# Kernel tuning notes

Hardware: AMD Instinct MI355X
Metric: run time of the kernel (lower is better)

## Reference

```python
import jax, jax.numpy as jnp
import numpy as np

N = 100000        # num nodes
E = 1200000       # num edges (avg degree 12)
F_IN = 64         # num_features
HID = 64          # hidden_size
NCLS = 40         # num_classes
K = 2             # propagation hops


def setup_inputs() -> dict:
    key = jax.random.key(0)
    k0, k1, k2, k3 = jax.random.split(key, 4)
    x = jax.random.normal(k0, (N, F_IN), dtype=jnp.float32)
    edge_index = jax.random.randint(k1, (2, E), 0, N, dtype=jnp.int32)
    # SGConv's internal Linear (in->hidden) and the classifier fc (hidden->classes)
    W1 = jax.random.normal(k2, (F_IN, HID), dtype=jnp.float32) / np.sqrt(F_IN).astype(np.float32)
    b1 = jnp.zeros((HID,), jnp.float32)
    W2 = jax.random.normal(k3, (HID, NCLS), dtype=jnp.float32) / np.sqrt(HID).astype(np.float32)
    b2 = jnp.zeros((NCLS,), jnp.float32)
    return {"x": x, "edge_index": edge_index, "W1": W1, "b1": b1, "W2": W2, "b2": b2}


def reference(x, edge_index, W1, b1, W2, b2):
    n = x.shape[0]
    # gcn_norm: add self-loops with weight 1, symmetric normalization
    loop = jnp.arange(n, dtype=edge_index.dtype)
    src = jnp.concatenate([edge_index[0], loop])  # message source j
    dst = jnp.concatenate([edge_index[1], loop])  # aggregation target i
    deg = jax.ops.segment_sum(jnp.ones(src.shape, x.dtype), dst, num_segments=n)
    dinv = jnp.where(deg > 0, jax.lax.rsqrt(deg), 0.0)
    norm = dinv[src] * dinv[dst]  # [E+N]
    # K-hop propagation: x_i <- sum_j norm_ij * x_j
    for _ in range(K):
        x = jax.ops.segment_sum(norm[:, None] * x[src], dst, num_segments=n)
    h = jax.nn.relu(x @ W1 + b1)          # SGConv lin + ReLU
    logits = h @ W2 + b2                  # fc
    return jax.nn.log_softmax(logits, axis=1)
```

## Files before the change

### kernel.cpp

```cpp
#include <hip/hip_runtime.h>
#include <math.h>

#define N_NODES 100000
#define BSHIFT 9
#define NBUCK 256
#define CAPSHIFT 13
#define CAP (1 << CAPSHIFT)

typedef unsigned short bfu;
typedef unsigned int uint;
typedef __attribute__((ext_vector_type(8))) short short8v;
typedef __attribute__((ext_vector_type(4))) float f32x4;
typedef __attribute__((ext_vector_type(2))) float f32x2;

__device__ __forceinline__ float bf2f(bfu u) {
    union { uint i; float f; } v; v.i = (uint)u << 16; return v.f;
}
__device__ __forceinline__ bfu f2bf(float f) {
    union { float f_; uint i; } v; v.f_ = f;
    uint r = (v.i + 0x7FFFu + ((v.i >> 16) & 1u)) >> 16;
    return (bfu)r;
}
__device__ __forceinline__ float asf(uint u) {
    union { uint i; float f; } v; v.i = u; return v.f;
}

__global__ __launch_bounds__(256) void bin_edges(const int* __restrict__ src,
                                                 const int* __restrict__ dst,
                                                 int* __restrict__ gcursor,
                                                 uint* __restrict__ binned, int nE) {
    __shared__ int h[NBUCK];
    __shared__ int base[NBUCK];
    int tid = threadIdx.x;
    int start = blockIdx.x * 4096;
    h[tid] = 0;
    __syncthreads();
    int bkt[16], rnk[16];
    #pragma unroll
    for (int u = 0; u < 16; ++u) {
        int e = start + u * 256 + tid;
        bkt[u] = -1;
        if (e < nE) {
            int b = dst[e] >> BSHIFT;
            bkt[u] = b;
            rnk[u] = atomicAdd(&h[b], 1);
        }
    }
    __syncthreads();
    base[tid] = h[tid] ? (tid << CAPSHIFT) + atomicAdd(&gcursor[tid], h[tid]) : 0;
    __syncthreads();
    #pragma unroll
    for (int u = 0; u < 16; ++u) {
        int e = start + u * 256 + tid;
        if (e < nE) {
            uint pk = ((uint)(dst[e] & 511) << 17) | (uint)src[e];
            binned[base[bkt[u]] + rnk[u]] = pk;
        }
    }
}

__global__ __launch_bounds__(512) void build_csr(
    const uint* __restrict__ binned, const int* __restrict__ gcursor,
    int* __restrict__ rowptr, int* __restrict__ rowend,
    float* __restrict__ dinv, int* __restrict__ nbr,
    const float4* __restrict__ x, ushort4* __restrict__ z0, int nN) {
    __shared__ int hist[512];
    __shared__ int cursor[512];
    int b = blockIdx.x, t = threadIdx.x;
    int n0 = b << BSHIFT;
    int nNodes = min(512, nN - n0);
    int base = b << CAPSHIFT;
    int cnt = gcursor[b];
    hist[t] = 0;
    __syncthreads();
    for (int i = t; i < cnt; i += 512)
        atomicAdd(&hist[binned[base + i] >> 17], 1);
    __syncthreads();
    int v = hist[t];
    #pragma unroll
    for (int off = 1; off < 512; off <<= 1) {
        int tv = (t >= off) ? hist[t - off] : 0;
        __syncthreads();
        hist[t] += tv;
        __syncthreads();
    }
    int excl = hist[t] - v;
    float dv = rsqrtf((float)v + 1.0f);
    if (t < nNodes) {
        rowptr[n0 + t] = base + excl;
        rowend[n0 + t] = base + excl + v;
        dinv[n0 + t] = dv;
    }
    cursor[t] = excl;
    __syncthreads();
    ((float*)hist)[t] = dv;
    __syncthreads();
    for (int i = t; i < cnt; i += 512) {
        uint pk = binned[base + i];
        int ld = pk >> 17;
        int pos = atomicAdd(&cursor[ld], 1);
        nbr[base + pos] = (int)(pk & 0x1FFFFu);
    }
    const float4* xr = x + (size_t)n0 * 16;
    ushort4* zr = z0 + (size_t)n0 * 16;
    int totalF4 = nNodes * 16;
    for (int i = t; i < totalF4; i += 512) {
        float w = ((float*)hist)[i >> 4];
        float4 vv = xr[i];
        ushort4 o;
        o.x = f2bf(w * vv.x); o.y = f2bf(w * vv.y);
        o.z = f2bf(w * vv.z); o.w = f2bf(w * vv.w);
        zr[i] = o;
    }
}

template<int PW>
__global__ __launch_bounds__(256, 8) void gather_hop8(
    bfu* __restrict__ out, const bfu* __restrict__ z,
    const int* __restrict__ nbr, const int* __restrict__ rowptr,
    const int* __restrict__ rowend, const float* __restrict__ dinv, int nN) {
    int node = blockIdx.x * 4 + (threadIdx.x >> 6);
    if (node >= nN) return;
    int lane = threadIdx.x & 63;
    int g = lane >> 3, k = lane & 7;
    int beg = rowptr[node], end = rowend[node];

    f32x2 a0 = {0.f, 0.f}, a1 = {0.f, 0.f}, a2 = {0.f, 0.f}, a3 = {0.f, 0.f};

    auto rowload = [&](int s) -> uint4 {
        return reinterpret_cast<const uint4*>(z + (size_t)s * 64)[k];
    };
    auto accum = [&](uint4 v) {
        f32x2 p;
        p.x = asf(v.x << 16); p.y = asf(v.x & 0xFFFF0000u); a0 += p;
        p.x = asf(v.y << 16); p.y = asf(v.y & 0xFFFF0000u); a1 += p;
        p.x = asf(v.z << 16); p.y = asf(v.z & 0xFFFF0000u); a2 += p;
        p.x = asf(v.w << 16); p.y = asf(v.w & 0xFFFF0000u); a3 += p;
    };

    if (g == 0)
        accum(rowload(node));
    int j = beg + g;
    for (; j + 8 < end; j += 16) {
        int i0 = nbr[j], i1 = nbr[j + 8];
        uint4 v0 = rowload(i0);
        uint4 v1 = rowload(i1);
        accum(v0);
        accum(v1);
    }
    if (j < end)
        accum(rowload(nbr[j]));

    float acc[8] = {a0.x, a0.y, a1.x, a1.y, a2.x, a2.y, a3.x, a3.y};
    #pragma unroll
    for (int m = 8; m < 64; m <<= 1)
        #pragma unroll
        for (int i = 0; i < 8; ++i)
            acc[i] += __shfl_xor(acc[i], m);

    if (g == 0) {
        float di = dinv[node];
        float w = (PW == 2) ? di * di : di;
        uint4 o;
        o.x = ((uint)f2bf(acc[1] * w) << 16) | f2bf(acc[0] * w);
        o.y = ((uint)f2bf(acc[3] * w) << 16) | f2bf(acc[2] * w);
        o.z = ((uint)f2bf(acc[5] * w) << 16) | f2bf(acc[4] * w);
        o.w = ((uint)f2bf(acc[7] * w) << 16) | f2bf(acc[6] * w);
        reinterpret_cast<uint4*>(out + (size_t)node * 64)[k] = o;
    }
}

__global__ __launch_bounds__(256) void mlp_mfma(
    float* __restrict__ out, const bfu* __restrict__ zC,
    const float* __restrict__ W1, const float* __restrict__ b1,
    const float* __restrict__ W2, const float* __restrict__ b2,
    int nN, int nTiles) {
    __shared__ short w1t[64 * 72];
    __shared__ short w2t[48 * 72];
    __shared__ short hlds[64 * 72];
    __shared__ float b1s[64];
    __shared__ float b2s[48];

    int tid = threadIdx.x;
    for (int i = tid; i < 64 * 64; i += 256) {
        int k = i >> 6, n = i & 63;
        w1t[n * 72 + k] = (short)f2bf(W1[i]);
    }
    for (int i = tid; i < 48 * 64; i += 256) {
        int k = i / 48, n = i % 48;
        w2t[n * 72 + k] = (short)(n < 40 ? f2bf(W2[k * 40 + n]) : 0);
    }
    if (tid < 64) b1s[tid] = b1[tid];
    if (tid >= 64 && tid < 112) b2s[tid - 64] = (tid - 64 < 40) ? b2[tid - 64] : 0.f;

    int wv = tid >> 6, l = tid & 63;
    int li = l & 15, kg = l >> 4;

    for (int tile = blockIdx.x; tile < nTiles; tile += gridDim.x) {
        int nodebase = tile * 64 + wv * 16;
        int nclamp = min(nodebase + li, nN - 1);

        const short8v* zr = (const short8v*)(zC + (size_t)nclamp * 64);
        short8v a0 = zr[kg];
        short8v a1 = zr[kg + 4];
        __syncthreads();

        f32x4 acc[4];
        #pragma unroll
        for (int nt = 0; nt < 4; ++nt) {
            f32x4 c = {0.f, 0.f, 0.f, 0.f};
            short8v b0 = *(const short8v*)&w1t[(nt * 16 + li) * 72 + kg * 8];
            short8v b1f = *(const short8v*)&w1t[(nt * 16 + li) * 72 + 32 + kg * 8];
            c = __builtin_amdgcn_mfma_f32_16x16x32_bf16(a0, b0, c, 0, 0, 0);
            c = __builtin_amdgcn_mfma_f32_16x16x32_bf16(a1, b1f, c, 0, 0, 0);
            acc[nt] = c;
        }
        #pragma unroll
        for (int nt = 0; nt < 4; ++nt) {
            float bb = b1s[nt * 16 + li];
            #pragma unroll
            for (int r = 0; r < 4; ++r) {
                float v = fmaxf(acc[nt][r] + bb, 0.f);
                hlds[(wv * 16 + kg * 4 + r) * 72 + nt * 16 + li] = (short)f2bf(v);
            }
        }
        __syncthreads();

        const short8v* hp = (const short8v*)&hlds[(wv * 16 + li) * 72];
        short8v ha0 = hp[kg];
        short8v ha1 = hp[kg + 4];
        f32x4 acc2[3];
        #pragma unroll
        for (int nt = 0; nt < 3; ++nt) {
            f32x4 c = {0.f, 0.f, 0.f, 0.f};
            short8v b0 = *(const short8v*)&w2t[(nt * 16 + li) * 72 + kg * 8];
            short8v b1f = *(const short8v*)&w2t[(nt * 16 + li) * 72 + 32 + kg * 8];
            c = __builtin_amdgcn_mfma_f32_16x16x32_bf16(ha0, b0, c, 0, 0, 0);
            c = __builtin_amdgcn_mfma_f32_16x16x32_bf16(ha1, b1f, c, 0, 0, 0);
            acc2[nt] = c;
        }

        float lg[3][4];
        #pragma unroll
        for (int nt = 0; nt < 3; ++nt) {
            float bb = b2s[nt * 16 + li];
            #pragma unroll
            for (int r = 0; r < 4; ++r) lg[nt][r] = acc2[nt][r] + bb;
        }
        bool v2 = (li < 8);
        float mx[4], sm[4];
        #pragma unroll
        for (int r = 0; r < 4; ++r) {
            float m = fmaxf(lg[0][r], lg[1][r]);
            if (v2) m = fmaxf(m, lg[2][r]);
            mx[r] = m;
        }
        #pragma unroll
        for (int off = 1; off < 16; off <<= 1)
            #pragma unroll
            for (int r = 0; r < 4; ++r)
                mx[r] = fmaxf(mx[r], __shfl_xor(mx[r], off));
        #pragma unroll
        for (int r = 0; r < 4; ++r) {
            float s = expf(lg[0][r] - mx[r]) + expf(lg[1][r] - mx[r]);
            if (v2) s += expf(lg[2][r] - mx[r]);
            sm[r] = s;
        }
        #pragma unroll
        for (int off = 1; off < 16; off <<= 1)
            #pragma unroll
            for (int r = 0; r < 4; ++r)
                sm[r] += __shfl_xor(sm[r], off);

        int nb2 = nodebase + kg * 4;
        #pragma unroll
        for (int r = 0; r < 4; ++r) {
            int nd = nb2 + r;
            if (nd < nN) {
                float lse = mx[r] + logf(sm[r]);
                out[(size_t)nd * 40 + li]      = lg[0][r] - lse;
                out[(size_t)nd * 40 + 16 + li] = lg[1][r] - lse;
                if (v2) out[(size_t)nd * 40 + 32 + li] = lg[2][r] - lse;
            }
        }
    }
}

extern "C" void kernel_launch(void* const* d_in, const int* in_sizes, int n_in,
                              void* d_out, int out_size, void* d_ws, size_t ws_size,
                              hipStream_t stream) {
    const float* x   = (const float*)d_in[0];
    const int* eidx  = (const int*)d_in[1];
    const float* W1  = (const float*)d_in[2];
    const float* b1  = (const float*)d_in[3];
    const float* W2  = (const float*)d_in[4];
    const float* b2  = (const float*)d_in[5];
    float* out = (float*)d_out;

    const int nN = N_NODES;
    const int nE = in_sizes[1] / 2;
    const int* src = eidx;
    const int* dst = eidx + nE;
    const int nBk = (nN + 511) >> BSHIFT;

    char* ws = (char*)d_ws;
    size_t off = 0;
    auto alloc = [&](size_t bytes) {
        char* p = ws + off;
        off += (bytes + 255) & ~(size_t)255;
        return p;
    };
    float* dinv    = (float*)alloc((size_t)nN * 4);
    int*   gcursor = (int*)  alloc(NBUCK * 4);
    int*   rowptr  = (int*)  alloc((size_t)nN * 4);
    int*   rowend  = (int*)  alloc((size_t)nN * 4);
    uint*  binned  = (uint*) alloc((size_t)NBUCK * CAP * 4);
    int*   nbr     = (int*)  alloc((size_t)NBUCK * CAP * 4);
    bfu*   z0      = (bfu*)  alloc((size_t)nN * 64 * 2);
    bfu*   zB      = (bfu*)  alloc((size_t)nN * 64 * 2);
    bfu*   zC      = (bfu*)  alloc((size_t)nN * 64 * 2);

    hipMemsetAsync(gcursor, 0, NBUCK * 4, stream);
    bin_edges<<<(nE + 4095) / 4096, 256, 0, stream>>>(src, dst, gcursor, binned, nE);
    build_csr<<<nBk, 512, 0, stream>>>(binned, gcursor, rowptr, rowend, dinv, nbr,
                                       (const float4*)x, (ushort4*)z0, nN);

    const int gBlocks = (nN + 3) / 4;
    gather_hop8<2><<<gBlocks, 256, 0, stream>>>(zB, z0, nbr, rowptr, rowend, dinv, nN);
    gather_hop8<1><<<gBlocks, 256, 0, stream>>>(zC, zB, nbr, rowptr, rowend, dinv, nN);

    const int nTiles = (nN + 63) / 64;
    mlp_mfma<<<392, 256, 0, stream>>>(out, zC, W1, b1, W2, b2, nN, nTiles);
}
```

Before: 144.5 us.

## Split features into column panels and gather per panel with XCD-aware mapping

```diff
diff --git a/kernel.cpp b/kernel.cpp
--- a/kernel.cpp
+++ b/kernel.cpp
@@ -63,7 +63,7 @@
     const uint* __restrict__ binned, const int* __restrict__ gcursor,
     int* __restrict__ rowptr, int* __restrict__ rowend,
     float* __restrict__ dinv, int* __restrict__ nbr,
-    const float4* __restrict__ x, ushort4* __restrict__ z0, int nN) {
+    const float4* __restrict__ x, bfu* __restrict__ z0, int nN) {
     __shared__ int hist[512];
     __shared__ int cursor[512];
     int b = blockIdx.x, t = threadIdx.x;
@@ -102,71 +102,63 @@
         nbr[base + pos] = (int)(pk & 0x1FFFFu);
     }
     const float4* xr = x + (size_t)n0 * 16;
-    ushort4* zr = z0 + (size_t)n0 * 16;
     int totalF4 = nNodes * 16;
     for (int i = t; i < totalF4; i += 512) {
-        float w = ((float*)hist)[i >> 4];
+        int n = i >> 4, f4 = i & 15;
+        float w = ((float*)hist)[n];
         float4 vv = xr[i];
         ushort4 o;
         o.x = f2bf(w * vv.x); o.y = f2bf(w * vv.y);
         o.z = f2bf(w * vv.z); o.w = f2bf(w * vv.w);
-        zr[i] = o;
+        *(ushort4*)(z0 + ((size_t)(f4 >> 2)) * nN * 16
+                       + (size_t)(n0 + n) * 16 + (f4 & 3) * 4) = o;
     }
 }
 
 template<int PW>
-__global__ __launch_bounds__(256, 8) void gather_hop8(
+__global__ __launch_bounds__(256, 8) void gather_panel(
     bfu* __restrict__ out, const bfu* __restrict__ z,
     const int* __restrict__ nbr, const int* __restrict__ rowptr,
     const int* __restrict__ rowend, const float* __restrict__ dinv, int nN) {
-    int node = blockIdx.x * 4 + (threadIdx.x >> 6);
-    if (node >= nN) return;
-    int lane = threadIdx.x & 63;
-    int g = lane >> 3, k = lane & 7;
-    int beg = rowptr[node], end = rowend[node];
-
-    f32x2 a0 = {0.f, 0.f}, a1 = {0.f, 0.f}, a2 = {0.f, 0.f}, a3 = {0.f, 0.f};
-
-    auto rowload = [&](int s) -> uint4 {
-        return reinterpret_cast<const uint4*>(z + (size_t)s * 64)[k];
-    };
-    auto accum = [&](uint4 v) {
-        f32x2 p;
-        p.x = asf(v.x << 16); p.y = asf(v.x & 0xFFFF0000u); a0 += p;
-        p.x = asf(v.y << 16); p.y = asf(v.y & 0xFFFF0000u); a1 += p;
-        p.x = asf(v.z << 16); p.y = asf(v.z & 0xFFFF0000u); a2 += p;
-        p.x = asf(v.w << 16); p.y = asf(v.w & 0xFFFF0000u); a3 += p;
-    };
-
-    if (g == 0)
-        accum(rowload(node));
-    int j = beg + g;
-    for (; j + 8 < end; j += 16) {
-        int i0 = nbr[j], i1 = nbr[j + 8];
-        uint4 v0 = rowload(i0);
-        uint4 v1 = rowload(i1);
-        accum(v0);
-        accum(v1);
-    }
-    if (j < end)
-        accum(rowload(nbr[j]));
-
-    float acc[8] = {a0.x, a0.y, a1.x, a1.y, a2.x, a2.y, a3.x, a3.y};
-    #pragma unroll
-    for (int m = 8; m < 64; m <<= 1)
-        #pragma unroll
-        for (int i = 0; i < 8; ++i)
-            acc[i] += __shfl_xor(acc[i], m);
-
-    if (g == 0) {
-        float di = dinv[node];
-        float w = (PW == 2) ? di * di : di;
-        uint4 o;
-        o.x = ((uint)f2bf(acc[1] * w) << 16) | f2bf(acc[0] * w);
-        o.y = ((uint)f2bf(acc[3] * w) << 16) | f2bf(acc[2] * w);
-        o.z = ((uint)f2bf(acc[5] * w) << 16) | f2bf(acc[4] * w);
-        o.w = ((uint)f2bf(acc[7] * w) << 16) | f2bf(acc[6] * w);
-        reinterpret_cast<uint4*>(out + (size_t)node * 64)[k] = o;
+    int b = blockIdx.x;
+    int panel = (b & 7) >> 1;
+    int chunk = ((b >> 3) << 1) | (b & 1);
+    int wv = threadIdx.x >> 6, lane = threadIdx.x & 63;
+    int e = lane >> 2, q = lane & 3;
+    const bfu* zp = z + (size_t)panel * nN * 16;
+    bfu* op = out + (size_t)panel * nN * 16;
+    int node0 = chunk * 64 + wv * 16;
+
+    for (int m = 0; m < 16; ++m) {
+        int node = node0 + m;
+        if (node >= nN) return;
+        int beg = rowptr[node], end = rowend[node];
+        f32x2 lo = {0.f, 0.f}, hi = {0.f, 0.f};
+        auto accum = [&](uint2 v) {
+            f32x2 p;
+            p.x = asf(v.x << 16); p.y = asf(v.x & 0xFFFF0000u); lo += p;
+            p.x = asf(v.y << 16); p.y = asf(v.y & 0xFFFF0000u); hi += p;
+        };
+        if (e == 0)
+            accum(*(const uint2*)(zp + (size_t)node * 16 + q * 4));
+        for (int j = beg + e; j < end; j += 16)
+            accum(*(const uint2*)(zp + (size_t)nbr[j] * 16 + q * 4));
+
+        float a[4] = {lo.x, lo.y, hi.x, hi.y};
+        #pragma unroll
+        for (int msk = 4; msk < 64; msk <<= 1)
+            #pragma unroll
+            for (int i = 0; i < 4; ++i)
+                a[i] += __shfl_xor(a[i], msk);
+
+        if (e == 0) {
+            float di = dinv[node];
+            float w = (PW == 2) ? di * di : di;
+            ushort4 o;
+            o.x = f2bf(a[0] * w); o.y = f2bf(a[1] * w);
+            o.z = f2bf(a[2] * w); o.w = f2bf(a[3] * w);
+            *(ushort4*)(op + (size_t)node * 16 + q * 4) = o;
+        }
     }
 }
 
@@ -200,9 +192,10 @@
         int nodebase = tile * 64 + wv * 16;
         int nclamp = min(nodebase + li, nN - 1);
 
-        const short8v* zr = (const short8v*)(zC + (size_t)nclamp * 64);
-        short8v a0 = zr[kg];
-        short8v a1 = zr[kg + 4];
+        short8v a0 = *(const short8v*)(zC + ((size_t)(kg >> 1)) * nN * 16
+                                          + (size_t)nclamp * 16 + (kg & 1) * 8);
+        short8v a1 = *(const short8v*)(zC + ((size_t)(2 + (kg >> 1))) * nN * 16
+                                          + (size_t)nclamp * 16 + (kg & 1) * 8);
         __syncthreads();
 
         f32x4 acc[4];
@@ -323,11 +316,11 @@
     hipMemsetAsync(gcursor, 0, NBUCK * 4, stream);
     bin_edges<<<(nE + 4095) / 4096, 256, 0, stream>>>(src, dst, gcursor, binned, nE);
     build_csr<<<nBk, 512, 0, stream>>>(binned, gcursor, rowptr, rowend, dinv, nbr,
-                                       (const float4*)x, (ushort4*)z0, nN);
-
-    const int gBlocks = (nN + 3) / 4;
-    gather_hop8<2><<<gBlocks, 256, 0, stream>>>(zB, z0, nbr, rowptr, rowend, dinv, nN);
-    gather_hop8<1><<<gBlocks, 256, 0, stream>>>(zC, zB, nbr, rowptr, rowend, dinv, nN);
+                                       (const float4*)x, z0, nN);
+
+    const int gGrid = 8 * 782;
+    gather_panel<2><<<gGrid, 256, 0, stream>>>(zB, z0, nbr, rowptr, rowend, dinv, nN);
+    gather_panel<1><<<gGrid, 256, 0, stream>>>(zC, zB, nbr, rowptr, rowend, dinv, nN);
 
     const int nTiles = (nN + 63) / 64;
     mlp_mfma<<<392, 256, 0, stream>>>(out, zC, W1, b1, W2, b2, nN, nTiles);
```

New measurement: 252.6 us. 74.7% more time.

## Fuse second propagation hop into the MLP kernel via shared-memory tile

Applied to the files above, without the earlier changes.

```diff
diff --git a/kernel.cpp b/kernel.cpp
--- a/kernel.cpp
+++ b/kernel.cpp
@@ -11,7 +11,6 @@
 typedef unsigned int uint;
 typedef __attribute__((ext_vector_type(8))) short short8v;
 typedef __attribute__((ext_vector_type(4))) float f32x4;
-typedef __attribute__((ext_vector_type(2))) float f32x2;
 
 __device__ __forceinline__ float bf2f(bfu u) {
     union { uint i; float f; } v; v.i = (uint)u << 16; return v.f;
@@ -125,17 +124,18 @@
     int g = lane >> 3, k = lane & 7;
     int beg = rowptr[node], end = rowend[node];
 
-    f32x2 a0 = {0.f, 0.f}, a1 = {0.f, 0.f}, a2 = {0.f, 0.f}, a3 = {0.f, 0.f};
+    float acc[8];
+    #pragma unroll
+    for (int i = 0; i < 8; ++i) acc[i] = 0.f;
 
     auto rowload = [&](int s) -> uint4 {
         return reinterpret_cast<const uint4*>(z + (size_t)s * 64)[k];
     };
     auto accum = [&](uint4 v) {
-        f32x2 p;
-        p.x = asf(v.x << 16); p.y = asf(v.x & 0xFFFF0000u); a0 += p;
-        p.x = asf(v.y << 16); p.y = asf(v.y & 0xFFFF0000u); a1 += p;
-        p.x = asf(v.z << 16); p.y = asf(v.z & 0xFFFF0000u); a2 += p;
-        p.x = asf(v.w << 16); p.y = asf(v.w & 0xFFFF0000u); a3 += p;
+        acc[0] += asf(v.x << 16); acc[1] += asf(v.x & 0xFFFF0000u);
+        acc[2] += asf(v.y << 16); acc[3] += asf(v.y & 0xFFFF0000u);
+        acc[4] += asf(v.z << 16); acc[5] += asf(v.z & 0xFFFF0000u);
+        acc[6] += asf(v.w << 16); acc[7] += asf(v.w & 0xFFFF0000u);
     };
 
     if (g == 0)
@@ -151,7 +151,6 @@
     if (j < end)
         accum(rowload(nbr[j]));
 
-    float acc[8] = {a0.x, a0.y, a1.x, a1.y, a2.x, a2.y, a3.x, a3.y};
     #pragma unroll
     for (int m = 8; m < 64; m <<= 1)
         #pragma unroll
@@ -170,14 +169,15 @@
     }
 }
 
-__global__ __launch_bounds__(256) void mlp_mfma(
-    float* __restrict__ out, const bfu* __restrict__ zC,
+__global__ __launch_bounds__(256) void hop2_mlp(
+    float* __restrict__ out, const bfu* __restrict__ zB,
+    const int* __restrict__ nbr, const int* __restrict__ rowptr,
+    const int* __restrict__ rowend, const float* __restrict__ dinv,
     const float* __restrict__ W1, const float* __restrict__ b1,
-    const float* __restrict__ W2, const float* __restrict__ b2,
-    int nN, int nTiles) {
+    const float* __restrict__ W2, const float* __restrict__ b2, int nN) {
     __shared__ short w1t[64 * 72];
     __shared__ short w2t[48 * 72];
-    __shared__ short hlds[64 * 72];
+    __shared__ short xh[64 * 72];
     __shared__ float b1s[64];
     __shared__ float b2s[48];
 
@@ -194,94 +194,125 @@
     if (tid >= 64 && tid < 112) b2s[tid - 64] = (tid - 64 < 40) ? b2[tid - 64] : 0.f;
 
     int wv = tid >> 6, l = tid & 63;
+    int g = l >> 3, k = l & 7;
+
+    auto rowload = [&](int s) -> uint4 {
+        return reinterpret_cast<const uint4*>(zB + (size_t)s * 64)[k];
+    };
+
+    int rowbase0 = blockIdx.x * 64 + wv * 16;
+    for (int m = 0; m < 16; ++m) {
+        int node = rowbase0 + m;
+        float acc[8];
+        #pragma unroll
+        for (int i = 0; i < 8; ++i) acc[i] = 0.f;
+        if (node < nN) {
+            int beg = rowptr[node], end = rowend[node];
+            auto accum = [&](uint4 v) {
+                acc[0] += asf(v.x << 16); acc[1] += asf(v.x & 0xFFFF0000u);
+                acc[2] += asf(v.y << 16); acc[3] += asf(v.y & 0xFFFF0000u);
+                acc[4] += asf(v.z << 16); acc[5] += asf(v.z & 0xFFFF0000u);
+                acc[6] += asf(v.w << 16); acc[7] += asf(v.w & 0xFFFF0000u);
+            };
+            if (g == 0) accum(rowload(node));
+            for (int j = beg + g; j < end; j += 8)
+                accum(rowload(nbr[j]));
+            #pragma unroll
+            for (int msk = 8; msk < 64; msk <<= 1)
+                #pragma unroll
+                for (int i = 0; i < 8; ++i)
+                    acc[i] += __shfl_xor(acc[i], msk);
+        }
+        if (g == 0) {
+            float w = (node < nN) ? dinv[node] : 0.f;
+            short8v o;
+            #pragma unroll
+            for (int i = 0; i < 8; ++i) o[i] = (short)f2bf(acc[i] * w);
+            *(short8v*)&xh[(wv * 16 + m) * 72 + k * 8] = o;
+        }
+    }
+    __syncthreads();
+
     int li = l & 15, kg = l >> 4;
-
-    for (int tile = blockIdx.x; tile < nTiles; tile += gridDim.x) {
-        int nodebase = tile * 64 + wv * 16;
-        int nclamp = min(nodebase + li, nN - 1);
-
-        const short8v* zr = (const short8v*)(zC + (size_t)nclamp * 64);
-        short8v a0 = zr[kg];
-        short8v a1 = zr[kg + 4];
-        __syncthreads();
-
-        f32x4 acc[4];
-        #pragma unroll
-        for (int nt = 0; nt < 4; ++nt) {
-            f32x4 c = {0.f, 0.f, 0.f, 0.f};
-            short8v b0 = *(const short8v*)&w1t[(nt * 16 + li) * 72 + kg * 8];
-            short8v b1f = *(const short8v*)&w1t[(nt * 16 + li) * 72 + 32 + kg * 8];
-            c = __builtin_amdgcn_mfma_f32_16x16x32_bf16(a0, b0, c, 0, 0, 0);
-            c = __builtin_amdgcn_mfma_f32_16x16x32_bf16(a1, b1f, c, 0, 0, 0);
-            acc[nt] = c;
-        }
-        #pragma unroll
-        for (int nt = 0; nt < 4; ++nt) {
-            float bb = b1s[nt * 16 + li];
-            #pragma unroll
-            for (int r = 0; r < 4; ++r) {
-                float v = fmaxf(acc[nt][r] + bb, 0.f);
-                hlds[(wv * 16 + kg * 4 + r) * 72 + nt * 16 + li] = (short)f2bf(v);
-            }
-        }
-        __syncthreads();
-
-        const short8v* hp = (const short8v*)&hlds[(wv * 16 + li) * 72];
-        short8v ha0 = hp[kg];
-        short8v ha1 = hp[kg + 4];
-        f32x4 acc2[3];
-        #pragma unroll
-        for (int nt = 0; nt < 3; ++nt) {
-            f32x4 c = {0.f, 0.f, 0.f, 0.f};
-            short8v b0 = *(const short8v*)&w2t[(nt * 16 + li) * 72 + kg * 8];
-            short8v b1f = *(const short8v*)&w2t[(nt * 16 + li) * 72 + 32 + kg * 8];
-            c = __builtin_amdgcn_mfma_f32_16x16x32_bf16(ha0, b0, c, 0, 0, 0);
-            c = __builtin_amdgcn_mfma_f32_16x16x32_bf16(ha1, b1f, c, 0, 0, 0);
-            acc2[nt] = c;
-        }
-
-        float lg[3][4];
-        #pragma unroll
-        for (int nt = 0; nt < 3; ++nt) {
-            float bb = b2s[nt * 16 + li];
-            #pragma unroll
-            for (int r = 0; r < 4; ++r) lg[nt][r] = acc2[nt][r] + bb;
-        }
-        bool v2 = (li < 8);
-        float mx[4], sm[4];
+    short8v a0 = *(const short8v*)&xh[(wv * 16 + li) * 72 + kg * 8];
+    short8v a1 = *(const short8v*)&xh[(wv * 16 + li) * 72 + 32 + kg * 8];
+    f32x4 acc1[4];
+    #pragma unroll
+    for (int nt = 0; nt < 4; ++nt) {
+        f32x4 c = {0.f, 0.f, 0.f, 0.f};
+        short8v b0 = *(const short8v*)&w1t[(nt * 16 + li) * 72 + kg * 8];
+        short8v b1f = *(const short8v*)&w1t[(nt * 16 + li) * 72 + 32 + kg * 8];
+        c = __builtin_amdgcn_mfma_f32_16x16x32_bf16(a0, b0, c, 0, 0, 0);
+        c = __builtin_amdgcn_mfma_f32_16x16x32_bf16(a1, b1f, c, 0, 0, 0);
+        acc1[nt] = c;
+    }
+    __syncthreads();
+    #pragma unroll
+    for (int nt = 0; nt < 4; ++nt) {
+        float bb = b1s[nt * 16 + li];
         #pragma unroll
         for (int r = 0; r < 4; ++r) {
-            float m = fmaxf(lg[0][r], lg[1][r]);
-            if (v2) m = fmaxf(m, lg[2][r]);
-            mx[r] = m;
-        }
-        #pragma unroll
-        for (int off = 1; off < 16; off <<= 1)
-            #pragma unroll
-            for (int r = 0; r < 4; ++r)
-                mx[r] = fmaxf(mx[r], __shfl_xor(mx[r], off));
-        #pragma unroll
-        for (int r = 0; r < 4; ++r) {
-            float s = expf(lg[0][r] - mx[r]) + expf(lg[1][r] - mx[r]);
-            if (v2) s += expf(lg[2][r] - mx[r]);
-            sm[r] = s;
-        }
-        #pragma unroll
-        for (int off = 1; off < 16; off <<= 1)
-            #pragma unroll
-            for (int r = 0; r < 4; ++r)
-                sm[r] += __shfl_xor(sm[r], off);
-
-        int nb2 = nodebase + kg * 4;
-        #pragma unroll
-        for (int r = 0; r < 4; ++r) {
-            int nd = nb2 + r;
-            if (nd < nN) {
-                float lse = mx[r] + logf(sm[r]);
-                out[(size_t)nd * 40 + li]      = lg[0][r] - lse;
-                out[(size_t)nd * 40 + 16 + li] = lg[1][r] - lse;
-                if (v2) out[(size_t)nd * 40 + 32 + li] = lg[2][r] - lse;
-            }
+            float v = fmaxf(acc1[nt][r] + bb, 0.f);
+            xh[(wv * 16 + kg * 4 + r) * 72 + nt * 16 + li] = (short)f2bf(v);
+        }
+    }
+    __syncthreads();
+
+    const short8v* hp = (const short8v*)&xh[(wv * 16 + li) * 72];
+    short8v ha0 = hp[kg];
+    short8v ha1 = hp[kg + 4];
+    f32x4 acc2[3];
+    #pragma unroll
+    for (int nt = 0; nt < 3; ++nt) {
+        f32x4 c = {0.f, 0.f, 0.f, 0.f};
+        short8v b0 = *(const short8v*)&w2t[(nt * 16 + li) * 72 + kg * 8];
+        short8v b1f = *(const short8v*)&w2t[(nt * 16 + li) * 72 + 32 + kg * 8];
+        c = __builtin_amdgcn_mfma_f32_16x16x32_bf16(ha0, b0, c, 0, 0, 0);
+        c = __builtin_amdgcn_mfma_f32_16x16x32_bf16(ha1, b1f, c, 0, 0, 0);
+        acc2[nt] = c;
+    }
+
+    float lg[3][4];
+    #pragma unroll
+    for (int nt = 0; nt < 3; ++nt) {
+        float bb = b2s[nt * 16 + li];
+        #pragma unroll
+        for (int r = 0; r < 4; ++r) lg[nt][r] = acc2[nt][r] + bb;
+    }
+    bool v2 = (li < 8);
+    float mx[4], sm[4];
+    #pragma unroll
+    for (int r = 0; r < 4; ++r) {
+        float m = fmaxf(lg[0][r], lg[1][r]);
+        if (v2) m = fmaxf(m, lg[2][r]);
+        mx[r] = m;
+    }
+    #pragma unroll
+    for (int off = 1; off < 16; off <<= 1)
+        #pragma unroll
+        for (int r = 0; r < 4; ++r)
+            mx[r] = fmaxf(mx[r], __shfl_xor(mx[r], off));
+    #pragma unroll
+    for (int r = 0; r < 4; ++r) {
+        float s = expf(lg[0][r] - mx[r]) + expf(lg[1][r] - mx[r]);
+        if (v2) s += expf(lg[2][r] - mx[r]);
+        sm[r] = s;
+    }
+    #pragma unroll
+    for (int off = 1; off < 16; off <<= 1)
+        #pragma unroll
+        for (int r = 0; r < 4; ++r)
+            sm[r] += __shfl_xor(sm[r], off);
+
+    int nb2 = blockIdx.x * 64 + wv * 16 + kg * 4;
+    #pragma unroll
+    for (int r = 0; r < 4; ++r) {
+        int nd = nb2 + r;
+        if (nd < nN) {
+            float lse = mx[r] + logf(sm[r]);
+            out[(size_t)nd * 40 + li]      = lg[0][r] - lse;
+            out[(size_t)nd * 40 + 16 + li] = lg[1][r] - lse;
+            if (v2) out[(size_t)nd * 40 + 32 + li] = lg[2][r] - lse;
         }
     }
 }
@@ -318,7 +349,6 @@
     int*   nbr     = (int*)  alloc((size_t)NBUCK * CAP * 4);
     bfu*   z0      = (bfu*)  alloc((size_t)nN * 64 * 2);
     bfu*   zB      = (bfu*)  alloc((size_t)nN * 64 * 2);
-    bfu*   zC      = (bfu*)  alloc((size_t)nN * 64 * 2);
 
     hipMemsetAsync(gcursor, 0, NBUCK * 4, stream);
     bin_edges<<<(nE + 4095) / 4096, 256, 0, stream>>>(src, dst, gcursor, binned, nE);
@@ -327,8 +357,7 @@
 
     const int gBlocks = (nN + 3) / 4;
     gather_hop8<2><<<gBlocks, 256, 0, stream>>>(zB, z0, nbr, rowptr, rowend, dinv, nN);
-    gather_hop8<1><<<gBlocks, 256, 0, stream>>>(zC, zB, nbr, rowptr, rowend, dinv, nN);
-
-    const int nTiles = (nN + 63) / 64;
-    mlp_mfma<<<392, 256, 0, stream>>>(out, zC, W1, b1, W2, b2, nN, nTiles);
-}
+
+    hop2_mlp<<<(nN + 63) / 64, 256, 0, stream>>>(out, zB, nbr, rowptr, rowend, dinv,
+                                                 W1, b1, W2, b2, nN);
+}
```

After: 170.4 us. 1.18x slower.
